# Performance work log

Hardware: AMD Instinct MI355X
Metric: run time of the kernel (lower is better)

Reference implementation:

```python
import jax, jax.numpy as jnp
import numpy as np

H = 256  # HIDDEN_SIZE
E = 256  # EMBED_SIZE
B = 128
L = 2048


def setup_inputs() -> dict:
    key = jax.random.key(0)
    ks = jax.random.split(key, 14)
    s = 1.0 / np.sqrt(H)
    return {
        "input_embed": jax.random.normal(ks[0], (B, 1, E), jnp.float32),
        "encoder_outputs": jax.random.normal(ks[1], (B, L, H), jnp.float32),
        "hidden1": jax.random.normal(ks[2], (1, B, H), jnp.float32),
        "cell1": jax.random.normal(ks[3], (1, B, H), jnp.float32),
        "hidden2": jax.random.normal(ks[4], (1, B, H), jnp.float32),
        "cell2": jax.random.normal(ks[5], (1, B, H), jnp.float32),
        "w_ih1": jax.random.normal(ks[6], (4 * H, H), jnp.float32) * s,
        "w_hh1": jax.random.normal(ks[7], (4 * H, H), jnp.float32) * s,
        "b_ih1": jax.random.normal(ks[8], (4 * H,), jnp.float32) * s,
        "b_hh1": jax.random.normal(ks[9], (4 * H,), jnp.float32) * s,
        "w_ih2": jax.random.normal(ks[10], (4 * H, E + H), jnp.float32) * s,
        "w_hh2": jax.random.normal(ks[11], (4 * H, H), jnp.float32) * s,
        "b_ih2": jax.random.normal(ks[12], (4 * H,), jnp.float32) * s,
        "b_hh2": jax.random.normal(ks[13], (4 * H,), jnp.float32) * s,
    }


def _lstm_step(x, h, c, w_ih, w_hh, b_ih, b_hh):
    # x: [B, D_in]; h, c: [B, H]. PyTorch gate order: i, f, g, o.
    gates = x @ w_ih.T + h @ w_hh.T + b_ih + b_hh  # [B, 4H]
    i, f, g, o = jnp.split(gates, 4, axis=-1)
    c_new = jax.nn.sigmoid(f) * c + jax.nn.sigmoid(i) * jnp.tanh(g)
    h_new = jax.nn.sigmoid(o) * jnp.tanh(c_new)
    return h_new, c_new


def reference(input_embed, encoder_outputs, hidden1, cell1, hidden2, cell2,
              w_ih1, w_hh1, b_ih1, b_hh1, w_ih2, w_hh2, b_ih2, b_hh2):
    # Attention: dot-product scores between hidden1[0] and each encoder step.
    scores = jnp.einsum('bh,blh->bl', hidden1[0], encoder_outputs)  # [B, L]
    alpha = jax.nn.softmax(scores, axis=1)
    context = jnp.einsum('bl,blh->bh', alpha, encoder_outputs)  # [B, H]

    # LSTM1 single step on the context vector.
    h1, c1 = _lstm_step(context, hidden1[0], cell1[0], w_ih1, w_hh1, b_ih1, b_hh1)
    mid = h1[:, None, :]  # [B, 1, H]

    # Concat embedding with LSTM1 output, run LSTM2 single step.
    new_mid = jnp.concatenate([input_embed[:, 0, :], h1], axis=-1)  # [B, E+H]
    h2, c2 = _lstm_step(new_mid, hidden2[0], cell2[0], w_ih2, w_hh2, b_ih2, b_hh2)
    outputs = h2[:, None, :]  # [B, 1, H]

    return (outputs, h1[None], c1[None], h2[None], c2[None])
```

## Files before the change

kernel.cpp:

```cpp
#include <hip/hip_runtime.h>
#include <math.h>

#define BN   128
#define LN   2048
#define HN   256
#define EN   256
#define CHUNKS 8
#define ROWS_PER_CHUNK (LN / CHUNKS)
#define PSTRIDE 260

__device__ __forceinline__ float sigmoidf_(float x) { return 1.0f / (1.0f + __expf(-x)); }
__device__ __forceinline__ float tanhf_(float x)    { return 1.0f - 2.0f / (__expf(2.0f * x) + 1.0f); }

__global__ __launch_bounds__(256) void attn_partial(
    const float* __restrict__ enc,
    const float* __restrict__ hidden1,
    float* __restrict__ partials)
{
    const int chunk = blockIdx.x;
    const int b     = blockIdx.y;
    const int t     = threadIdx.x;
    const int wave  = t >> 6;
    const int lane  = t & 63;

    __shared__ float lds_ctx[4][256];
    __shared__ float lds_m[4], lds_s[4];

    const float4 h4 = *(const float4*)(hidden1 + b * HN + lane * 4);

    float  m = -INFINITY, s = 0.0f;
    float4 ctx = make_float4(0.f, 0.f, 0.f, 0.f);

    const float* rowp = enc + ((size_t)b * LN + (size_t)chunk * ROWS_PER_CHUNK + wave * 64) * HN + lane * 4;

    #pragma unroll 2
    for (int r = 0; r < 64; ++r) {
        float4 e = *(const float4*)rowp;
        rowp += HN;
        float d = e.x * h4.x + e.y * h4.y + e.z * h4.z + e.w * h4.w;
        #pragma unroll
        for (int off = 32; off > 0; off >>= 1) d += __shfl_xor(d, off, 64);
        float mn   = fmaxf(m, d);
        float corr = __expf(m - mn);
        float p    = __expf(d - mn);
        s = s * corr + p;
        ctx.x = ctx.x * corr + p * e.x;
        ctx.y = ctx.y * corr + p * e.y;
        ctx.z = ctx.z * corr + p * e.z;
        ctx.w = ctx.w * corr + p * e.w;
        m = mn;
    }

    *(float4*)&lds_ctx[wave][lane * 4] = ctx;
    if (lane == 0) { lds_m[wave] = m; lds_s[wave] = s; }
    __syncthreads();

    float M = fmaxf(fmaxf(lds_m[0], lds_m[1]), fmaxf(lds_m[2], lds_m[3]));
    float e0 = __expf(lds_m[0] - M), e1 = __expf(lds_m[1] - M);
    float e2 = __expf(lds_m[2] - M), e3 = __expf(lds_m[3] - M);
    float cj = e0 * lds_ctx[0][t] + e1 * lds_ctx[1][t] + e2 * lds_ctx[2][t] + e3 * lds_ctx[3][t];
    float S  = e0 * lds_s[0] + e1 * lds_s[1] + e2 * lds_s[2] + e3 * lds_s[3];

    float* pb = partials + ((size_t)b * CHUNKS + chunk) * PSTRIDE;
    pb[t] = cj;
    if (t == 0) { pb[256] = M; pb[257] = S; }
}

__global__ __launch_bounds__(256) void combine_prep(
    const float* __restrict__ partials,
    const float* __restrict__ hidden1,
    const float* __restrict__ embed,
    const float* __restrict__ hidden2,
    float* __restrict__ xh1,
    float* __restrict__ xh2)
{
    const int b = blockIdx.x;
    const int j = threadIdx.x;
    const float* pb = partials + (size_t)b * CHUNKS * PSTRIDE;

    float mk[CHUNKS], sk[CHUNKS];
    float M = -INFINITY;
    #pragma unroll
    for (int k = 0; k < CHUNKS; ++k) {
        mk[k] = pb[k * PSTRIDE + 256];
        sk[k] = pb[k * PSTRIDE + 257];
        M = fmaxf(M, mk[k]);
    }
    float S = 0.0f, cj = 0.0f;
    #pragma unroll
    for (int k = 0; k < CHUNKS; ++k) {
        float e = __expf(mk[k] - M);
        S  += e * sk[k];
        cj += e * pb[k * PSTRIDE + j];
    }
    cj /= S;

    xh1[b * 512 + j]       = cj;
    xh1[b * 512 + 256 + j] = hidden1[b * HN + j];
    xh2[b * 768 + j]       = embed[b * EN + j];
    xh2[b * 768 + 512 + j] = hidden2[b * HN + j];
}

__global__ __launch_bounds__(128) void lstm1_kernel(
    const float* __restrict__ xh,
    const float* __restrict__ w_ih,
    const float* __restrict__ w_hh,
    const float* __restrict__ b_ih,
    const float* __restrict__ b_hh,
    const float* __restrict__ cell,
    float* __restrict__ h_out,
    float* __restrict__ c_out,
    float* __restrict__ xh2)
{
    __shared__ float wq[512 * 32];
    const int t  = threadIdx.x;
    const int jb = blockIdx.x;
    const int bb = blockIdx.y;

    #pragma unroll 4
    for (int it = 0; it < 32; ++it) {
        int idx  = (it * 128 + t) * 4;
        int row  = idx >> 9;
        int k0   = idx & 511;
        int q    = row >> 3, jl = row & 7;
        int g    = q * 256 + jb * 8 + jl;
        float4 v = (k0 < 256) ? *(const float4*)(w_ih + (size_t)g * 256 + k0)
                              : *(const float4*)(w_hh + (size_t)g * 256 + (k0 - 256));
        wq[(k0 + 0) * 32 + jl * 4 + q] = v.x;
        wq[(k0 + 1) * 32 + jl * 4 + q] = v.y;
        wq[(k0 + 2) * 32 + jl * 4 + q] = v.z;
        wq[(k0 + 3) * 32 + jl * 4 + q] = v.w;
    }
    __syncthreads();

    const int jl = t & 7, bl = t >> 3;
    const int b = bb * 16 + bl;
    const int j = jb * 8 + jl;

    float acc0 = 0.f, acc1 = 0.f, acc2 = 0.f, acc3 = 0.f;
    const float* xr = xh + (size_t)b * 512;
    #pragma unroll 4
    for (int k4 = 0; k4 < 128; ++k4) {
        float4 xv = *(const float4*)(xr + k4 * 4);
        #pragma unroll
        for (int i = 0; i < 4; ++i) {
            float xe = (i == 0) ? xv.x : (i == 1) ? xv.y : (i == 2) ? xv.z : xv.w;
            float4 w4 = *(float4*)&wq[(k4 * 4 + i) * 32 + jl * 4];
            acc0 += w4.x * xe; acc1 += w4.y * xe; acc2 += w4.z * xe; acc3 += w4.w * xe;
        }
    }

    float gi = acc0 + b_ih[j]       + b_hh[j];
    float gf = acc1 + b_ih[256 + j] + b_hh[256 + j];
    float gg = acc2 + b_ih[512 + j] + b_hh[512 + j];
    float go = acc3 + b_ih[768 + j] + b_hh[768 + j];

    float cp = cell[b * HN + j];
    float cn = sigmoidf_(gf) * cp + sigmoidf_(gi) * tanhf_(gg);
    float hn = sigmoidf_(go) * tanhf_(cn);

    c_out[b * HN + j] = cn;
    h_out[b * HN + j] = hn;
    xh2[b * 768 + 256 + j] = hn;
}

__global__ __launch_bounds__(128) void lstm2_kernel(
    const float* __restrict__ xh,
    const float* __restrict__ w_ih,
    const float* __restrict__ w_hh,
    const float* __restrict__ b_ih,
    const float* __restrict__ b_hh,
    const float* __restrict__ cell,
    float* __restrict__ out0,
    float* __restrict__ h_out,
    float* __restrict__ c_out)
{
    __shared__ float wq[768 * 16];
    const int t  = threadIdx.x;
    const int jb = blockIdx.x;
    const int bb = blockIdx.y;

    #pragma unroll 4
    for (int it = 0; it < 24; ++it) {
        int idx = (it * 128 + t) * 4;
        int row = idx / 768;
        int k0  = idx - row * 768;
        int q   = row >> 2, jl = row & 3;
        int g   = q * 256 + jb * 4 + jl;
        float4 v = (k0 < 512) ? *(const float4*)(w_ih + (size_t)g * 512 + k0)
                              : *(const float4*)(w_hh + (size_t)g * 256 + (k0 - 512));
        wq[(k0 + 0) * 16 + jl * 4 + q] = v.x;
        wq[(k0 + 1) * 16 + jl * 4 + q] = v.y;
        wq[(k0 + 2) * 16 + jl * 4 + q] = v.z;
        wq[(k0 + 3) * 16 + jl * 4 + q] = v.w;
    }
    __syncthreads();

    const int jl = t & 3, bl = t >> 2;
    const int b = bb * 32 + bl;
    const int j = jb * 4 + jl;

    float acc0 = 0.f, acc1 = 0.f, acc2 = 0.f, acc3 = 0.f;
    const float* xr = xh + (size_t)b * 768;
    #pragma unroll 4
    for (int k4 = 0; k4 < 192; ++k4) {
        float4 xv = *(const float4*)(xr + k4 * 4);
        #pragma unroll
        for (int i = 0; i < 4; ++i) {
            float xe = (i == 0) ? xv.x : (i == 1) ? xv.y : (i == 2) ? xv.z : xv.w;
            float4 w4 = *(float4*)&wq[(k4 * 4 + i) * 16 + jl * 4];
            acc0 += w4.x * xe; acc1 += w4.y * xe; acc2 += w4.z * xe; acc3 += w4.w * xe;
        }
    }

    float gi = acc0 + b_ih[j]       + b_hh[j];
    float gf = acc1 + b_ih[256 + j] + b_hh[256 + j];
    float gg = acc2 + b_ih[512 + j] + b_hh[512 + j];
    float go = acc3 + b_ih[768 + j] + b_hh[768 + j];

    float cp = cell[b * HN + j];
    float cn = sigmoidf_(gf) * cp + sigmoidf_(gi) * tanhf_(gg);
    float hn = sigmoidf_(go) * tanhf_(cn);

    out0[b * HN + j]  = hn;
    h_out[b * HN + j] = hn;
    c_out[b * HN + j] = cn;
}

extern "C" void kernel_launch(void* const* d_in, const int* in_sizes, int n_in,
                              void* d_out, int out_size, void* d_ws, size_t ws_size,
                              hipStream_t stream)
{
    const float* embed   = (const float*)d_in[0];
    const float* enc     = (const float*)d_in[1];
    const float* hidden1 = (const float*)d_in[2];
    const float* cell1   = (const float*)d_in[3];
    const float* hidden2 = (const float*)d_in[4];
    const float* cell2   = (const float*)d_in[5];
    const float* w_ih1   = (const float*)d_in[6];
    const float* w_hh1   = (const float*)d_in[7];
    const float* b_ih1   = (const float*)d_in[8];
    const float* b_hh1   = (const float*)d_in[9];
    const float* w_ih2   = (const float*)d_in[10];
    const float* w_hh2   = (const float*)d_in[11];
    const float* b_ih2   = (const float*)d_in[12];
    const float* b_hh2   = (const float*)d_in[13];

    float* out = (float*)d_out;
    float* ws = (float*)d_ws;
    float* partials = ws;
    float* xh1 = ws + (size_t)BN * CHUNKS * PSTRIDE;
    float* xh2 = xh1 + (size_t)BN * 512;

    attn_partial<<<dim3(CHUNKS, BN), 256, 0, stream>>>(enc, hidden1, partials);
    combine_prep<<<dim3(BN), 256, 0, stream>>>(partials, hidden1, embed, hidden2, xh1, xh2);
    lstm1_kernel<<<dim3(32, 8), 128, 0, stream>>>(xh1, w_ih1, w_hh1, b_ih1, b_hh1, cell1,
                                                  out + 32768, out + 65536, xh2);
    lstm2_kernel<<<dim3(64, 4), 128, 0, stream>>>(xh2, w_ih2, w_hh2, b_ih2, b_hh2, cell2,
                                                  out, out + 98304, out + 131072);
}
```

Measured before the change: 434.3 us.

## Batch attention rows per softmax update and restructure LSTM weight staging

Result: no change. 442.9 us (+2.0%).

```diff
diff --git a/kernel.cpp b/kernel.cpp
--- a/kernel.cpp
+++ b/kernel.cpp
@@ -6,7 +6,6 @@
 #define HN   256
 #define EN   256
 #define CHUNKS 8
-#define ROWS_PER_CHUNK (LN / CHUNKS)
 #define PSTRIDE 260
 
 __device__ __forceinline__ float sigmoidf_(float x) { return 1.0f / (1.0f + __expf(-x)); }
@@ -31,23 +30,41 @@
     float  m = -INFINITY, s = 0.0f;
     float4 ctx = make_float4(0.f, 0.f, 0.f, 0.f);
 
-    const float* rowp = enc + ((size_t)b * LN + (size_t)chunk * ROWS_PER_CHUNK + wave * 64) * HN + lane * 4;
-
-    #pragma unroll 2
-    for (int r = 0; r < 64; ++r) {
-        float4 e = *(const float4*)rowp;
-        rowp += HN;
-        float d = e.x * h4.x + e.y * h4.y + e.z * h4.z + e.w * h4.w;
-        #pragma unroll
-        for (int off = 32; off > 0; off >>= 1) d += __shfl_xor(d, off, 64);
-        float mn   = fmaxf(m, d);
+    const float* rowp = enc + ((size_t)b * LN + (size_t)chunk * 256 + wave * 64) * HN + lane * 4;
+
+    for (int batch = 0; batch < 8; ++batch) {
+        float4 e[8];
+        float  d[8];
+        #pragma unroll
+        for (int r = 0; r < 8; ++r) {
+            e[r] = *(const float4*)(rowp + r * HN);
+            d[r] = e[r].x * h4.x + e[r].y * h4.y + e[r].z * h4.z + e[r].w * h4.w;
+        }
+        rowp += 8 * HN;
+        #pragma unroll
+        for (int off = 1; off < 64; off <<= 1) {
+            #pragma unroll
+            for (int r = 0; r < 8; ++r) d[r] += __shfl_xor(d[r], off, 64);
+        }
+        float dmax = d[0];
+        #pragma unroll
+        for (int r = 1; r < 8; ++r) dmax = fmaxf(dmax, d[r]);
+        float mn   = fmaxf(m, dmax);
         float corr = __expf(m - mn);
-        float p    = __expf(d - mn);
-        s = s * corr + p;
-        ctx.x = ctx.x * corr + p * e.x;
-        ctx.y = ctx.y * corr + p * e.y;
-        ctx.z = ctx.z * corr + p * e.z;
-        ctx.w = ctx.w * corr + p * e.w;
+        float psum = 0.0f;
+        float4 add = make_float4(0.f, 0.f, 0.f, 0.f);
+        #pragma unroll
+        for (int r = 0; r < 8; ++r) {
+            float p = __expf(d[r] - mn);
+            psum  += p;
+            add.x += p * e[r].x; add.y += p * e[r].y;
+            add.z += p * e[r].z; add.w += p * e[r].w;
+        }
+        s = s * corr + psum;
+        ctx.x = ctx.x * corr + add.x;
+        ctx.y = ctx.y * corr + add.y;
+        ctx.z = ctx.z * corr + add.z;
+        ctx.w = ctx.w * corr + add.w;
         m = mn;
     }
 
@@ -112,56 +129,69 @@
     float* __restrict__ c_out,
     float* __restrict__ xh2)
 {
-    __shared__ float wq[512 * 32];
+    __shared__ float wq[32 * 512];
     const int t  = threadIdx.x;
     const int jb = blockIdx.x;
     const int bb = blockIdx.y;
 
-    #pragma unroll 4
-    for (int it = 0; it < 32; ++it) {
-        int idx  = (it * 128 + t) * 4;
-        int row  = idx >> 9;
-        int k0   = idx & 511;
-        int q    = row >> 3, jl = row & 7;
-        int g    = q * 256 + jb * 8 + jl;
-        float4 v = (k0 < 256) ? *(const float4*)(w_ih + (size_t)g * 256 + k0)
-                              : *(const float4*)(w_hh + (size_t)g * 256 + (k0 - 256));
-        wq[(k0 + 0) * 32 + jl * 4 + q] = v.x;
-        wq[(k0 + 1) * 32 + jl * 4 + q] = v.y;
-        wq[(k0 + 2) * 32 + jl * 4 + q] = v.z;
-        wq[(k0 + 3) * 32 + jl * 4 + q] = v.w;
+    #pragma unroll 16
+    for (int row = 0; row < 32; ++row) {
+        int q  = row >> 3, jl = row & 7;
+        int g  = q * 256 + jb * 8 + jl;
+        int k  = t * 4;
+        float4 v = (k < 256) ? *(const float4*)(w_ih + (size_t)g * 256 + k)
+                             : *(const float4*)(w_hh + (size_t)g * 256 + (k - 256));
+        int cp = (t + row) & 127;
+        *(float4*)&wq[row * 512 + cp * 4] = v;
     }
     __syncthreads();
 
     const int jl = t & 7, bl = t >> 3;
-    const int b = bb * 16 + bl;
-    const int j = jb * 8 + jl;
-
-    float acc0 = 0.f, acc1 = 0.f, acc2 = 0.f, acc3 = 0.f;
-    const float* xr = xh + (size_t)b * 512;
-    #pragma unroll 4
+    const int b0 = bb * 32 + bl, b1 = b0 + 16;
+    const int j  = jb * 8 + jl;
+
+    float accA[4] = {0.f, 0.f, 0.f, 0.f};
+    float accB[4] = {0.f, 0.f, 0.f, 0.f};
+    const float* xra = xh + (size_t)b0 * 512;
+    const float* xrb = xh + (size_t)b1 * 512;
+
+    #pragma unroll 8
     for (int k4 = 0; k4 < 128; ++k4) {
-        float4 xv = *(const float4*)(xr + k4 * 4);
-        #pragma unroll
-        for (int i = 0; i < 4; ++i) {
-            float xe = (i == 0) ? xv.x : (i == 1) ? xv.y : (i == 2) ? xv.z : xv.w;
-            float4 w4 = *(float4*)&wq[(k4 * 4 + i) * 32 + jl * 4];
-            acc0 += w4.x * xe; acc1 += w4.y * xe; acc2 += w4.z * xe; acc3 += w4.w * xe;
-        }
-    }
-
-    float gi = acc0 + b_ih[j]       + b_hh[j];
-    float gf = acc1 + b_ih[256 + j] + b_hh[256 + j];
-    float gg = acc2 + b_ih[512 + j] + b_hh[512 + j];
-    float go = acc3 + b_ih[768 + j] + b_hh[768 + j];
-
-    float cp = cell[b * HN + j];
-    float cn = sigmoidf_(gf) * cp + sigmoidf_(gi) * tanhf_(gg);
-    float hn = sigmoidf_(go) * tanhf_(cn);
-
-    c_out[b * HN + j] = cn;
-    h_out[b * HN + j] = hn;
-    xh2[b * 768 + 256 + j] = hn;
+        float4 xa = *(const float4*)(xra + k4 * 4);
+        float4 xb = *(const float4*)(xrb + k4 * 4);
+        #pragma unroll
+        for (int q = 0; q < 4; ++q) {
+            int row = q * 8 + jl;
+            float4 w4 = *(float4*)&wq[row * 512 + ((k4 + row) & 127) * 4];
+            accA[q] += w4.x * xa.x + w4.y * xa.y + w4.z * xa.z + w4.w * xa.w;
+            accB[q] += w4.x * xb.x + w4.y * xb.y + w4.z * xb.z + w4.w * xb.w;
+        }
+    }
+
+    float bias[4];
+    #pragma unroll
+    for (int q = 0; q < 4; ++q) bias[q] = b_ih[q * 256 + j] + b_hh[q * 256 + j];
+
+    {
+        float gi = accA[0] + bias[0], gf = accA[1] + bias[1];
+        float gg = accA[2] + bias[2], go = accA[3] + bias[3];
+        float cp = cell[b0 * HN + j];
+        float cn = sigmoidf_(gf) * cp + sigmoidf_(gi) * tanhf_(gg);
+        float hn = sigmoidf_(go) * tanhf_(cn);
+        c_out[b0 * HN + j] = cn;
+        h_out[b0 * HN + j] = hn;
+        xh2[b0 * 768 + 256 + j] = hn;
+    }
+    {
+        float gi = accB[0] + bias[0], gf = accB[1] + bias[1];
+        float gg = accB[2] + bias[2], go = accB[3] + bias[3];
+        float cp = cell[b1 * HN + j];
+        float cn = sigmoidf_(gf) * cp + sigmoidf_(gi) * tanhf_(gg);
+        float hn = sigmoidf_(go) * tanhf_(cn);
+        c_out[b1 * HN + j] = cn;
+        h_out[b1 * HN + j] = hn;
+        xh2[b1 * 768 + 256 + j] = hn;
+    }
 }
 
 __global__ __launch_bounds__(128) void lstm2_kernel(
@@ -175,56 +205,86 @@
     float* __restrict__ h_out,
     float* __restrict__ c_out)
 {
-    __shared__ float wq[768 * 16];
+    __shared__ float wA[16 * 512];
+    __shared__ float wB[16 * 256];
     const int t  = threadIdx.x;
     const int jb = blockIdx.x;
     const int bb = blockIdx.y;
 
-    #pragma unroll 4
-    for (int it = 0; it < 24; ++it) {
-        int idx = (it * 128 + t) * 4;
-        int row = idx / 768;
-        int k0  = idx - row * 768;
+    #pragma unroll 16
+    for (int row = 0; row < 16; ++row) {
+        int q  = row >> 2, jl = row & 3;
+        int g  = q * 256 + jb * 4 + jl;
+        float4 v = *(const float4*)(w_ih + (size_t)g * 512 + t * 4);
+        int cp = (t + row) & 127;
+        *(float4*)&wA[row * 512 + cp * 4] = v;
+    }
+    #pragma unroll 8
+    for (int it = 0; it < 8; ++it) {
+        int row = it * 2 + (t >> 6);
+        int c   = t & 63;
         int q   = row >> 2, jl = row & 3;
         int g   = q * 256 + jb * 4 + jl;
-        float4 v = (k0 < 512) ? *(const float4*)(w_ih + (size_t)g * 512 + k0)
-                              : *(const float4*)(w_hh + (size_t)g * 256 + (k0 - 512));
-        wq[(k0 + 0) * 16 + jl * 4 + q] = v.x;
-        wq[(k0 + 1) * 16 + jl * 4 + q] = v.y;
-        wq[(k0 + 2) * 16 + jl * 4 + q] = v.z;
-        wq[(k0 + 3) * 16 + jl * 4 + q] = v.w;
+        float4 v = *(const float4*)(w_hh + (size_t)g * 256 + c * 4);
+        int cp = (c + row) & 63;
+        *(float4*)&wB[row * 256 + cp * 4] = v;
     }
     __syncthreads();
 
     const int jl = t & 3, bl = t >> 2;
-    const int b = bb * 32 + bl;
-    const int j = jb * 4 + jl;
-
-    float acc0 = 0.f, acc1 = 0.f, acc2 = 0.f, acc3 = 0.f;
-    const float* xr = xh + (size_t)b * 768;
-    #pragma unroll 4
-    for (int k4 = 0; k4 < 192; ++k4) {
-        float4 xv = *(const float4*)(xr + k4 * 4);
-        #pragma unroll
-        for (int i = 0; i < 4; ++i) {
-            float xe = (i == 0) ? xv.x : (i == 1) ? xv.y : (i == 2) ? xv.z : xv.w;
-            float4 w4 = *(float4*)&wq[(k4 * 4 + i) * 16 + jl * 4];
-            acc0 += w4.x * xe; acc1 += w4.y * xe; acc2 += w4.z * xe; acc3 += w4.w * xe;
-        }
-    }
-
-    float gi = acc0 + b_ih[j]       + b_hh[j];
-    float gf = acc1 + b_ih[256 + j] + b_hh[256 + j];
-    float gg = acc2 + b_ih[512 + j] + b_hh[512 + j];
-    float go = acc3 + b_ih[768 + j] + b_hh[768 + j];
-
-    float cp = cell[b * HN + j];
-    float cn = sigmoidf_(gf) * cp + sigmoidf_(gi) * tanhf_(gg);
-    float hn = sigmoidf_(go) * tanhf_(cn);
-
-    out0[b * HN + j]  = hn;
-    h_out[b * HN + j] = hn;
-    c_out[b * HN + j] = cn;
+    const int b0 = bb * 64 + bl, b1 = b0 + 32;
+    const int j  = jb * 4 + jl;
+
+    float accA[4] = {0.f, 0.f, 0.f, 0.f};
+    float accB[4] = {0.f, 0.f, 0.f, 0.f};
+    const float* xra = xh + (size_t)b0 * 768;
+    const float* xrb = xh + (size_t)b1 * 768;
+
+    #pragma unroll 8
+    for (int k4 = 0; k4 < 128; ++k4) {
+        float4 xa = *(const float4*)(xra + k4 * 4);
+        float4 xb = *(const float4*)(xrb + k4 * 4);
+        #pragma unroll
+        for (int q = 0; q < 4; ++q) {
+            int row = q * 4 + jl;
+            float4 w4 = *(float4*)&wA[row * 512 + ((k4 + row) & 127) * 4];
+            accA[q] += w4.x * xa.x + w4.y * xa.y + w4.z * xa.z + w4.w * xa.w;
+            accB[q] += w4.x * xb.x + w4.y * xb.y + w4.z * xb.z + w4.w * xb.w;
+        }
+    }
+    #pragma unroll 8
+    for (int k4 = 0; k4 < 64; ++k4) {
+        float4 xa = *(const float4*)(xra + 512 + k4 * 4);
+        float4 xb = *(const float4*)(xrb + 512 + k4 * 4);
+        #pragma unroll
+        for (int q = 0; q < 4; ++q) {
+            int row = q * 4 + jl;
+            float4 w4 = *(float4*)&wB[row * 256 + ((k4 + row) & 63) * 4];
+            accA[q] += w4.x * xa.x + w4.y * xa.y + w4.z * xa.z + w4.w * xa.w;
+            accB[q] += w4.x * xb.x + w4.y * xb.y + w4.z * xb.z + w4.w * xb.w;
+        }
+    }
+
+    float bias[4];
+    #pragma unroll
+    for (int q = 0; q < 4; ++q) bias[q] = b_ih[q * 256 + j] + b_hh[q * 256 + j];
+
+    {
+        float gi = accA[0] + bias[0], gf = accA[1] + bias[1];
+        float gg = accA[2] + bias[2], go = accA[3] + bias[3];
+        float cp = cell[b0 * HN + j];
+        float cn = sigmoidf_(gf) * cp + sigmoidf_(gi) * tanhf_(gg);
+        float hn = sigmoidf_(go) * tanhf_(cn);
+        out0[b0 * HN + j] = hn; h_out[b0 * HN + j] = hn; c_out[b0 * HN + j] = cn;
+    }
+    {
+        float gi = accB[0] + bias[0], gf = accB[1] + bias[1];
+        float gg = accB[2] + bias[2], go = accB[3] + bias[3];
+        float cp = cell[b1 * HN + j];
+        float cn = sigmoidf_(gf) * cp + sigmoidf_(gi) * tanhf_(gg);
+        float hn = sigmoidf_(go) * tanhf_(cn);
+        out0[b1 * HN + j] = hn; h_out[b1 * HN + j] = hn; c_out[b1 * HN + j] = cn;
+    }
 }
 
 extern "C" void kernel_launch(void* const* d_in, const int* in_sizes, int n_in,
@@ -254,8 +314,8 @@
 
     attn_partial<<<dim3(CHUNKS, BN), 256, 0, stream>>>(enc, hidden1, partials);
     combine_prep<<<dim3(BN), 256, 0, stream>>>(partials, hidden1, embed, hidden2, xh1, xh2);
-    lstm1_kernel<<<dim3(32, 8), 128, 0, stream>>>(xh1, w_ih1, w_hh1, b_ih1, b_hh1, cell1,
+    lstm1_kernel<<<dim3(32, 4), 128, 0, stream>>>(xh1, w_ih1, w_hh1, b_ih1, b_hh1, cell1,
                                                   out + 32768, out + 65536, xh2);
-    lstm2_kernel<<<dim3(64, 4), 128, 0, stream>>>(xh2, w_ih2, w_hh2, b_ih2, b_hh2, cell2,
+    lstm2_kernel<<<dim3(64, 2), 128, 0, stream>>>(xh2, w_ih2, w_hh2, b_ih2, b_hh2, cell2,
                                                   out, out + 98304, out + 131072);
 }
```
